# Optimization experiments

Hardware: AMD Instinct MI355X
Metric: run time of the kernel (lower is better)

Reference implementation:

```python
import jax, jax.numpy as jnp
import numpy as np

DIM = 32
DEPTH = 2  # closed-form Lyndon-basis log-signature implemented for depth 2


def setup_inputs() -> dict:
    key = jax.random.key(0)
    B, L, D = 512, 2048, DIM
    x = jax.random.normal(key, (B, L, D), dtype=jnp.float32)
    return {"x": x}


def _logsig_depth2(x):
    # x: (B, L, D) batch of paths.
    dx = x[:, 1:, :] - x[:, :-1, :]                     # (B, L-1, D) increments
    prefix = jnp.cumsum(dx, axis=1)                      # inclusive prefix sums
    level1 = prefix[:, -1, :]                            # (B, D) total displacement
    prefix_excl = prefix - dx                            # prefix up to t-1 (exclusive)
    # level-2 signature S_ij = sum_t prefix_excl[t, i] * dx[t, j]  -> (B, D, D)
    S2 = jnp.einsum("bli,blj->bij", prefix_excl, dx)
    # log-signature level 2 = antisymmetric part (Levy areas), Lyndon words i<j
    A = 0.5 * (S2 - jnp.swapaxes(S2, 1, 2))             # (B, D, D)
    iu, ju = jnp.triu_indices(x.shape[-1], k=1)          # row-major upper triangle
    areas = A[:, iu, ju]                                 # (B, D*(D-1)/2)
    return jnp.concatenate([level1, areas], axis=-1)     # (B, D + D*(D-1)/2)


def reference(x):
    # Faithful batched equivalent of iisignature.logsig(path, prepare(dim, 2))
    # for every path in the batch (Lyndon basis, depth 2).
    return _logsig_depth2(x)
```

## Files before the change

### kernel.cpp

```cpp
#include <hip/hip_runtime.h>
#include <stdint.h>


constexpr int kB     = 512;
constexpr int kL     = 2048;
constexpr int kD     = 32;
constexpr int kOut   = 528;
constexpr int kTw    = 256;
constexpr int kPan   = 32;
constexpr int kSlot  = 36;

typedef __attribute__((ext_vector_type(8))) short bfrag;
typedef __attribute__((ext_vector_type(4))) float f4acc;

union FragU { uint32_t u[4]; bfrag f; };

__device__ __forceinline__ uint32_t bf16_rne(float f) {
    uint32_t fb = __builtin_bit_cast(uint32_t, f);
    return (fb + 0x7fffu + ((fb >> 16) & 1u)) >> 16;
}

__global__ __launch_bounds__(256, 4)
void logsig_mfma(const float* __restrict__ x, float* __restrict__ out) {
    __shared__ __align__(16) uint32_t xp[4][kD * kSlot];
    __shared__ float sM[kD * kD];
    __shared__ float sx0[kD], sL1[kD];

    const int b     = blockIdx.x >> 1;
    const int halfc = blockIdx.x & 1;
    const int tid   = threadIdx.x;
    const int wave  = tid >> 6;
    const int lane  = tid & 63;

    const float* __restrict__ xb = x + (size_t)b * (kL * kD);
    const int t0 = (halfc * 4 + wave) * kTw;

    uint32_t* wbuf = &xp[wave][0];

    const int srow = lane >> 3;
    const int sd0  = (lane & 7) * 4;

    f4acc acc[4];
    #pragma unroll
    for (int t = 0; t < 4; ++t)
        #pragma unroll
        for (int e = 0; e < 4; ++e) acc[t][e] = 0.0f;

    auto load_panel = [&](int p, float4* G) {
        #pragma unroll
        for (int s = 0; s < 5; ++s) {
            const int r = s * 8 + srow;
            int row = t0 + p * kPan + r;
            row = row < kL - 1 ? row : kL - 1;
            if (r < 33)
                G[s] = *(const float4*)(xb + (size_t)row * kD + sd0);
        }
    };

    auto store_panel = [&](const float4* G) {
        #pragma unroll
        for (int s = 0; s < 5; ++s) {
            const int r = s * 8 + srow;
            if (r < 33) {
                const float v[4] = {G[s].x, G[s].y, G[s].z, G[s].w};
                #pragma unroll
                for (int k = 0; k < 4; ++k) {
                    const float f = v[k];
                    const uint32_t hi = bf16_rne(f);
                    const float fh = __builtin_bit_cast(float, hi << 16);
                    const uint32_t lo = bf16_rne(f - fh);
                    wbuf[(sd0 + k) * kSlot + r] = (hi & 0xffffu) | (lo << 16);
                }
            }
        }
    };

    const int m = lane & 15;
    const int q = lane >> 4;

    auto panel_compute = [&](void) {
        const uint32_t* r0 = wbuf + m * kSlot + q * 8;
        const uint32_t* r1 = wbuf + (m + 16) * kSlot + q * 8;
        const uint4 a0l = *(const uint4*)(r0);
        const uint4 a0h = *(const uint4*)(r0 + 4);
        const uint4 a1l = *(const uint4*)(r1);
        const uint4 a1h = *(const uint4*)(r1 + 4);
        const uint32_t a0[8] = {a0l.x, a0l.y, a0l.z, a0l.w, a0h.x, a0h.y, a0h.z, a0h.w};
        const uint32_t a1[8] = {a1l.x, a1l.y, a1l.z, a1l.w, a1h.x, a1h.y, a1h.z, a1h.w};
        uint32_t b0[8], b1[8];
        #pragma unroll
        for (int j = 0; j < 8; ++j) { b0[j] = r0[j + 1]; b1[j] = r1[j + 1]; }

        FragU A0H, A0L, A1H, A1L, B0H, B0L, B1H, B1L;
        #pragma unroll
        for (int j = 0; j < 4; ++j) {
            A0H.u[j] = __builtin_amdgcn_perm(a0[2*j+1], a0[2*j], 0x05040100u);
            A0L.u[j] = __builtin_amdgcn_perm(a0[2*j+1], a0[2*j], 0x07060302u);
            A1H.u[j] = __builtin_amdgcn_perm(a1[2*j+1], a1[2*j], 0x05040100u);
            A1L.u[j] = __builtin_amdgcn_perm(a1[2*j+1], a1[2*j], 0x07060302u);
            B0H.u[j] = __builtin_amdgcn_perm(b0[2*j+1], b0[2*j], 0x05040100u);
            B0L.u[j] = __builtin_amdgcn_perm(b0[2*j+1], b0[2*j], 0x07060302u);
            B1H.u[j] = __builtin_amdgcn_perm(b1[2*j+1], b1[2*j], 0x05040100u);
            B1L.u[j] = __builtin_amdgcn_perm(b1[2*j+1], b1[2*j], 0x07060302u);
        }
        acc[0] = __builtin_amdgcn_mfma_f32_16x16x32_bf16(A0H.f, B0H.f, acc[0], 0, 0, 0);
        acc[0] = __builtin_amdgcn_mfma_f32_16x16x32_bf16(A0H.f, B0L.f, acc[0], 0, 0, 0);
        acc[0] = __builtin_amdgcn_mfma_f32_16x16x32_bf16(A0L.f, B0H.f, acc[0], 0, 0, 0);
        acc[1] = __builtin_amdgcn_mfma_f32_16x16x32_bf16(A0H.f, B1H.f, acc[1], 0, 0, 0);
        acc[1] = __builtin_amdgcn_mfma_f32_16x16x32_bf16(A0H.f, B1L.f, acc[1], 0, 0, 0);
        acc[1] = __builtin_amdgcn_mfma_f32_16x16x32_bf16(A0L.f, B1H.f, acc[1], 0, 0, 0);
        acc[2] = __builtin_amdgcn_mfma_f32_16x16x32_bf16(A1H.f, B0H.f, acc[2], 0, 0, 0);
        acc[2] = __builtin_amdgcn_mfma_f32_16x16x32_bf16(A1H.f, B0L.f, acc[2], 0, 0, 0);
        acc[2] = __builtin_amdgcn_mfma_f32_16x16x32_bf16(A1L.f, B0H.f, acc[2], 0, 0, 0);
        acc[3] = __builtin_amdgcn_mfma_f32_16x16x32_bf16(A1H.f, B1H.f, acc[3], 0, 0, 0);
        acc[3] = __builtin_amdgcn_mfma_f32_16x16x32_bf16(A1H.f, B1L.f, acc[3], 0, 0, 0);
        acc[3] = __builtin_amdgcn_mfma_f32_16x16x32_bf16(A1L.f, B1H.f, acc[3], 0, 0, 0);
    };

    float4 G[5];
    load_panel(0, G);
    store_panel(G);
    for (int p = 0; p < kTw / kPan; ++p) {
        float4 Gn[5];
        if (p < kTw / kPan - 1) load_panel(p + 1, Gn);
        panel_compute();
        if (p < kTw / kPan - 1) store_panel(Gn);
    }

    for (int c = tid; c < kD * kD; c += 256) sM[c] = 0.0f;
    if (tid < kD) {
        const float x0v = xb[tid];
        const float xev = xb[(size_t)(kL - 1) * kD + tid];
        sx0[tid] = x0v;
        sL1[tid] = xev - x0v;
    }
    __syncthreads();

    #pragma unroll
    for (int t = 0; t < 4; ++t) {
        const int tr = t >> 1, tc = t & 1;
        #pragma unroll
        for (int e = 0; e < 4; ++e) {
            const int row = 16 * tr + q * 4 + e;
            const int col = 16 * tc + m;
            atomicAdd(&sM[row * kD + col], acc[t][e]);
        }
    }
    __syncthreads();

    float* ob = out + (size_t)b * kOut;
    for (int o = tid; o < kOut; o += 256) {
        if (o < 32) {
            if (halfc == 0) ob[o] = sL1[o];
        } else {
            int p = o - 32, i = 0;
            while (p >= 31 - i) { p -= 31 - i; ++i; }
            const int j = i + 1 + p;
            float v = 0.5f * (sM[i * kD + j] - sM[j * kD + i]);
            if (halfc == 0)
                v += 0.5f * (sx0[j] * sL1[i] - sx0[i] * sL1[j]);
            atomicAdd(ob + o, v);
        }
    }
}

extern "C" void kernel_launch(void* const* d_in, const int* in_sizes, int n_in,
                              void* d_out, int out_size, void* d_ws, size_t ws_size,
                              hipStream_t stream) {
    const float* x = (const float*)d_in[0];
    float* out = (float*)d_out;
    hipMemsetAsync(out, 0, (size_t)out_size * sizeof(float), stream);
    logsig_mfma<<<dim3(kB * 2), dim3(256), 0, stream>>>(x, out);
}
```

Baseline: 210.4 us.

## Load MFMA fragments directly from global memory, dropping LDS staging

Each lane now loads its fragment elements straight from global memory in MFMA layout, with scalar strided loads, instead of staging transposed bf16 hi/lo pairs through per-wave shared memory. The hi part is now made by truncation rather than round-to-nearest, and the lo residual is computed in registers. This removes the LDS writes and reads and the rounding arithmetic. In exchange, the global loads are uncoalesced 4-byte loads (16 lanes touch consecutive dwords), and truncation slightly changes the numerical error.

```diff
diff --git a/kernel.cpp b/kernel.cpp
--- a/kernel.cpp
+++ b/kernel.cpp
@@ -2,27 +2,20 @@
 #include <stdint.h>
 
 
-constexpr int kB     = 512;
-constexpr int kL     = 2048;
-constexpr int kD     = 32;
-constexpr int kOut   = 528;
-constexpr int kTw    = 256;
-constexpr int kPan   = 32;
-constexpr int kSlot  = 36;
+constexpr int kB   = 512;
+constexpr int kL   = 2048;
+constexpr int kD   = 32;
+constexpr int kOut = 528;
+constexpr int kTw  = 256;
+constexpr int kPan = 32;
+constexpr int kNP  = kTw / kPan;
 
 typedef __attribute__((ext_vector_type(8))) short bfrag;
 typedef __attribute__((ext_vector_type(4))) float f4acc;
-
 union FragU { uint32_t u[4]; bfrag f; };
-
-__device__ __forceinline__ uint32_t bf16_rne(float f) {
-    uint32_t fb = __builtin_bit_cast(uint32_t, f);
-    return (fb + 0x7fffu + ((fb >> 16) & 1u)) >> 16;
-}
 
 __global__ __launch_bounds__(256, 4)
 void logsig_mfma(const float* __restrict__ x, float* __restrict__ out) {
-    __shared__ __align__(16) uint32_t xp[4][kD * kSlot];
     __shared__ float sM[kD * kD];
     __shared__ float sx0[kD], sL1[kD];
 
@@ -31,14 +24,15 @@
     const int tid   = threadIdx.x;
     const int wave  = tid >> 6;
     const int lane  = tid & 63;
+    const int m     = lane & 15;
+    const int q     = lane >> 4;
 
     const float* __restrict__ xb = x + (size_t)b * (kL * kD);
     const int t0 = (halfc * 4 + wave) * kTw;
+    const int rb0 = t0 + q * 8;
 
-    uint32_t* wbuf = &xp[wave][0];
-
-    const int srow = lane >> 3;
-    const int sd0  = (lane & 7) * 4;
+    const uint32_t* __restrict__ base =
+        (const uint32_t*)xb + (size_t)rb0 * kD + m;
 
     f4acc acc[4];
     #pragma unroll
@@ -46,63 +40,49 @@
         #pragma unroll
         for (int e = 0; e < 4; ++e) acc[t][e] = 0.0f;
 
-    auto load_panel = [&](int p, float4* G) {
+    auto load_panel = [&](int p, uint32_t* e0, uint32_t* e1) {
+        const uint32_t* bp = base + (size_t)p * kPan * kD;
         #pragma unroll
-        for (int s = 0; s < 5; ++s) {
-            const int r = s * 8 + srow;
-            int row = t0 + p * kPan + r;
-            row = row < kL - 1 ? row : kL - 1;
-            if (r < 33)
-                G[s] = *(const float4*)(xb + (size_t)row * kD + sd0);
+        for (int j = 0; j < 8; ++j) {
+            e0[j] = bp[j * kD];
+            e1[j] = bp[j * kD + 16];
+        }
+        const int rb = rb0 + p * kPan;
+        const int ex = (rb + 8 <= kL - 1 ? 8 : (kL - 1) - rb) * kD;
+        e0[8] = bp[ex];
+        e1[8] = bp[ex + 16];
+    };
+
+    auto make_frags = [&](const uint32_t* e, FragU& AH, FragU& AL,
+                          FragU& BH, FragU& BL) {
+        uint32_t l[9];
+        #pragma unroll
+        for (int j = 0; j < 9; ++j) {
+            const uint32_t fh = e[j] & 0xffff0000u;
+            const float r = __builtin_bit_cast(float, e[j])
+                          - __builtin_bit_cast(float, fh);
+            l[j] = __builtin_bit_cast(uint32_t, r);
+        }
+        #pragma unroll
+        for (int d = 0; d < 4; ++d) {
+            AH.u[d] = __builtin_amdgcn_perm(e[2*d+1], e[2*d],   0x07060302u);
+            AL.u[d] = __builtin_amdgcn_perm(l[2*d+1], l[2*d],   0x07060302u);
+            BH.u[d] = __builtin_amdgcn_perm(e[2*d+2], e[2*d+1], 0x07060302u);
+            BL.u[d] = __builtin_amdgcn_perm(l[2*d+2], l[2*d+1], 0x07060302u);
         }
     };
 
-    auto store_panel = [&](const float4* G) {
-        #pragma unroll
-        for (int s = 0; s < 5; ++s) {
-            const int r = s * 8 + srow;
-            if (r < 33) {
-                const float v[4] = {G[s].x, G[s].y, G[s].z, G[s].w};
-                #pragma unroll
-                for (int k = 0; k < 4; ++k) {
-                    const float f = v[k];
-                    const uint32_t hi = bf16_rne(f);
-                    const float fh = __builtin_bit_cast(float, hi << 16);
-                    const uint32_t lo = bf16_rne(f - fh);
-                    wbuf[(sd0 + k) * kSlot + r] = (hi & 0xffffu) | (lo << 16);
-                }
-            }
-        }
-    };
+    uint32_t cur0[9], cur1[9], nxt0[9], nxt1[9];
+    load_panel(0, cur0, cur1);
 
-    const int m = lane & 15;
-    const int q = lane >> 4;
+    #pragma unroll
+    for (int p = 0; p < kNP; ++p) {
+        if (p + 1 < kNP) load_panel(p + 1, nxt0, nxt1);
 
-    auto panel_compute = [&](void) {
-        const uint32_t* r0 = wbuf + m * kSlot + q * 8;
-        const uint32_t* r1 = wbuf + (m + 16) * kSlot + q * 8;
-        const uint4 a0l = *(const uint4*)(r0);
-        const uint4 a0h = *(const uint4*)(r0 + 4);
-        const uint4 a1l = *(const uint4*)(r1);
-        const uint4 a1h = *(const uint4*)(r1 + 4);
-        const uint32_t a0[8] = {a0l.x, a0l.y, a0l.z, a0l.w, a0h.x, a0h.y, a0h.z, a0h.w};
-        const uint32_t a1[8] = {a1l.x, a1l.y, a1l.z, a1l.w, a1h.x, a1h.y, a1h.z, a1h.w};
-        uint32_t b0[8], b1[8];
-        #pragma unroll
-        for (int j = 0; j < 8; ++j) { b0[j] = r0[j + 1]; b1[j] = r1[j + 1]; }
+        FragU A0H, A0L, B0H, B0L, A1H, A1L, B1H, B1L;
+        make_frags(cur0, A0H, A0L, B0H, B0L);
+        make_frags(cur1, A1H, A1L, B1H, B1L);
 
-        FragU A0H, A0L, A1H, A1L, B0H, B0L, B1H, B1L;
-        #pragma unroll
-        for (int j = 0; j < 4; ++j) {
-            A0H.u[j] = __builtin_amdgcn_perm(a0[2*j+1], a0[2*j], 0x05040100u);
-            A0L.u[j] = __builtin_amdgcn_perm(a0[2*j+1], a0[2*j], 0x07060302u);
-            A1H.u[j] = __builtin_amdgcn_perm(a1[2*j+1], a1[2*j], 0x05040100u);
-            A1L.u[j] = __builtin_amdgcn_perm(a1[2*j+1], a1[2*j], 0x07060302u);
-            B0H.u[j] = __builtin_amdgcn_perm(b0[2*j+1], b0[2*j], 0x05040100u);
-            B0L.u[j] = __builtin_amdgcn_perm(b0[2*j+1], b0[2*j], 0x07060302u);
-            B1H.u[j] = __builtin_amdgcn_perm(b1[2*j+1], b1[2*j], 0x05040100u);
-            B1L.u[j] = __builtin_amdgcn_perm(b1[2*j+1], b1[2*j], 0x07060302u);
-        }
         acc[0] = __builtin_amdgcn_mfma_f32_16x16x32_bf16(A0H.f, B0H.f, acc[0], 0, 0, 0);
         acc[0] = __builtin_amdgcn_mfma_f32_16x16x32_bf16(A0H.f, B0L.f, acc[0], 0, 0, 0);
         acc[0] = __builtin_amdgcn_mfma_f32_16x16x32_bf16(A0L.f, B0H.f, acc[0], 0, 0, 0);
@@ -115,16 +95,9 @@
         acc[3] = __builtin_amdgcn_mfma_f32_16x16x32_bf16(A1H.f, B1H.f, acc[3], 0, 0, 0);
         acc[3] = __builtin_amdgcn_mfma_f32_16x16x32_bf16(A1H.f, B1L.f, acc[3], 0, 0, 0);
         acc[3] = __builtin_amdgcn_mfma_f32_16x16x32_bf16(A1L.f, B1H.f, acc[3], 0, 0, 0);
-    };
 
-    float4 G[5];
-    load_panel(0, G);
-    store_panel(G);
-    for (int p = 0; p < kTw / kPan; ++p) {
-        float4 Gn[5];
-        if (p < kTw / kPan - 1) load_panel(p + 1, Gn);
-        panel_compute();
-        if (p < kTw / kPan - 1) store_panel(Gn);
+        #pragma unroll
+        for (int j = 0; j < 9; ++j) { cur0[j] = nxt0[j]; cur1[j] = nxt1[j]; }
     }
 
     for (int c = tid; c < kD * kD; c += 256) sM[c] = 0.0f;
```

Result: no change. 208.6 us (-0.8%).
